# Kernel tuning notes

Measured on AMD Instinct MI355X. Metric: run time of the kernel, lower is better.

Reference implementation:

```python
import jax, jax.numpy as jnp
import numpy as np

HIDDEN = 512
NHEADS = 8
ALPHA = 0.1
NUM_HOP = 4
MASK_VAL = -16384.0
LN_EPS = 1e-5


def setup_inputs() -> dict:
    key = jax.random.key(0)
    ks = jax.random.split(key, 10)
    B, N, H = 8, 1024, HIDDEN
    s = 1.0 / np.sqrt(H)
    x = jax.random.normal(ks[0], (B, N, H), dtype=jnp.float32)
    adj = jax.random.randint(ks[1], (B, N, N), 0, 2, dtype=jnp.int32)
    Wq = jax.random.uniform(ks[2], (H, H), jnp.float32, -s, s)
    bq = jax.random.uniform(ks[3], (H,), jnp.float32, -s, s)
    Wk = jax.random.uniform(ks[4], (H, H), jnp.float32, -s, s)
    bk = jax.random.uniform(ks[5], (H,), jnp.float32, -s, s)
    Wv = jax.random.uniform(ks[6], (H, H), jnp.float32, -s, s)
    bv = jax.random.uniform(ks[7], (H,), jnp.float32, -s, s)
    gamma = jnp.ones((H,), jnp.float32)
    beta = jnp.zeros((H,), jnp.float32)
    return {"x": x, "adj": adj, "Wq": Wq, "bq": bq, "Wk": Wk, "bk": bk,
            "Wv": Wv, "bv": bv, "gamma": gamma, "beta": beta}


def reference(x, adj, Wq, bq, Wk, bk, Wv, bv, gamma, beta):
    B, N, H = x.shape
    u = H // NHEADS
    # torch Linear: y = x @ W^T + b
    q = x @ Wq.T + bq  # [B,N,H]
    k = x @ Wk.T + bk
    v = x @ Wv.T + bv
    # split hidden into contiguous head chunks (matches per-head slicing)
    qh = q.reshape(B, N, NHEADS, u).transpose(0, 2, 1, 3)  # [B,Hd,N,u]
    kh = k.reshape(B, N, NHEADS, u).transpose(0, 2, 1, 3)
    vh = v.reshape(B, N, NHEADS, u).transpose(0, 2, 1, 3)
    scores = jnp.einsum('bhnd,bhmd->bhnm', qh, kh)  # [B,Hd,N,N]
    mask = (adj == 0)[:, None, :, :]  # broadcast over heads
    scores = jnp.where(mask, MASK_VAL, scores)
    pros = jax.nn.softmax(scores, axis=-1)
    z_init = vh
    z = z_init
    for _ in range(NUM_HOP):
        z = (1.0 - ALPHA) * jnp.einsum('bhnm,bhmd->bhnd', pros, z) + ALPHA * z_init
    h_prime = z.transpose(0, 2, 1, 3).reshape(B, N, H)  # concat heads
    y = x + h_prime
    mu = jnp.mean(y, axis=-1, keepdims=True)
    var = jnp.mean((y - mu) ** 2, axis=-1, keepdims=True)
    return (y - mu) / jnp.sqrt(var + LN_EPS) * gamma + beta
```

## Files before the change

### kernel.cpp

```cpp
#include <hip/hip_runtime.h>
#include <hip/hip_bf16.h>

#define BB 8
#define NN 1024
#define HH 512
#define NHEADS 8
#define UU 64

typedef __attribute__((ext_vector_type(8))) short short8;
typedef __attribute__((ext_vector_type(4))) float f32x4;
typedef __attribute__((ext_vector_type(16))) float f32x16;
typedef unsigned short u16;
typedef unsigned char u8;

__device__ inline float b2f(unsigned short u) {
    union { float f; unsigned int i; } c; c.i = ((unsigned int)u) << 16; return c.f;
}
__device__ inline unsigned short f2b(float f) {
    __hip_bfloat16 h = __float2bfloat16(f);
    return *reinterpret_cast<unsigned short*>(&h);
}
__device__ inline unsigned int pkbf(float a, float b) {
    union { float f; unsigned int u; } ca, cb; ca.f = a; cb.f = b;
    return ((ca.u + 0x8000u) >> 16) | ((cb.u + 0x8000u) & 0xffff0000u);
}
__device__ inline float upk_lo(unsigned int u) {
    union { float f; unsigned int i; } c; c.i = u << 16; return c.f;
}
__device__ inline float upk_hi(unsigned int u) {
    union { float f; unsigned int i; } c; c.i = u & 0xffff0000u; return c.f;
}
__device__ inline void gl_lds16(const void* g, void* l) {
    __builtin_amdgcn_global_load_lds(
        (const __attribute__((address_space(1))) unsigned int*)g,
        (__attribute__((address_space(3))) unsigned int*)l, 16, 0, 0);
}

__global__ __launch_bounds__(256) void cvt_w(
    const float* __restrict__ Wq, const float* __restrict__ Wk,
    const float* __restrict__ Wv, u16* __restrict__ Wb)
{
    const int which = blockIdx.y;
    const float* src = which == 0 ? Wq : (which == 1 ? Wk : Wv);
    u16* dst = Wb + (size_t)which * HH * HH;
    const int base = (blockIdx.x * 256 + threadIdx.x) * 8;
    const float4* sp = (const float4*)&src[base];
    float4 a = sp[0], b = sp[1];
    short8 o;
    o[0] = (short)f2b(a.x); o[1] = (short)f2b(a.y);
    o[2] = (short)f2b(a.z); o[3] = (short)f2b(a.w);
    o[4] = (short)f2b(b.x); o[5] = (short)f2b(b.y);
    o[6] = (short)f2b(b.z); o[7] = (short)f2b(b.w);
    *(short8*)&dst[base] = o;
}

__global__ __launch_bounds__(256) void adj_pack(
    const int* __restrict__ adj, unsigned int* __restrict__ adjpT)
{
    const int wave = threadIdx.x >> 6, lane = threadIdx.x & 63;
    const int row = blockIdx.x * 4 + wave;
    const int b = row >> 10, r = row & 1023;
    const int* ar = adj + (size_t)row * NN;
    unsigned int* ob = adjpT + (((size_t)b) << 15) + r;
    #pragma unroll
    for (int it = 0; it < 16; ++it) {
        int a = ar[it * 64 + lane];
        unsigned long long m = __ballot(a != 0);
        if (lane == 0) {
            ob[(size_t)(2 * it)     << 10] = (unsigned int)m;
            ob[(size_t)(2 * it + 1) << 10] = (unsigned int)(m >> 32);
        }
    }
}

__global__ __launch_bounds__(256) void qkv_gemm(
    const float* __restrict__ x, const u16* __restrict__ Wb,
    const float* __restrict__ bq, const float* __restrict__ bk,
    const float* __restrict__ bv,
    u16* __restrict__ q, u16* __restrict__ k, u16* __restrict__ v)
{
    const int which = blockIdx.z;
    const u16* W      = Wb + (size_t)which * HH * HH;
    const float* bias = which == 0 ? bq : (which == 1 ? bk : bv);
    u16* out          = which == 0 ? q  : (which == 1 ? k  : v);

    const int tid = threadIdx.x;
    const int wave = tid >> 6, lane = tid & 63;
    const int ln = lane & 15, quad = lane >> 4;
    const int wr = (wave >> 1) * 64, wc = (wave & 1) * 64;
    const int rowbase = blockIdx.x * 128, colbase = blockIdx.y * 128;

    __shared__ __align__(16) u16 As[128 * 40];
    __shared__ __align__(16) u16 Bs[128 * 32];
    __shared__ __align__(16) u16 Cs[128 * 136];

    f32x4 acc[4][4];
    #pragma unroll
    for (int ri = 0; ri < 4; ++ri)
        #pragma unroll
        for (int ci = 0; ci < 4; ++ci) acc[ri][ci] = (f32x4){0.f, 0.f, 0.f, 0.f};

    const int lr = lane >> 2;
    const int sg = lane & 3;

    for (int kk = 0; kk < HH; kk += 32) {
        __syncthreads();
        #pragma unroll
        for (int i = 0; i < 2; ++i) {
            int r = wave * 32 + i * 16 + lr;
            const float* xp = &x[(size_t)(rowbase + r) * HH + kk + sg * 8];
            float4 f0 = *(const float4*)xp, f1 = *(const float4*)(xp + 4);
            short8 o;
            o[0] = (short)f2b(f0.x); o[1] = (short)f2b(f0.y);
            o[2] = (short)f2b(f0.z); o[3] = (short)f2b(f0.w);
            o[4] = (short)f2b(f1.x); o[5] = (short)f2b(f1.y);
            o[6] = (short)f2b(f1.z); o[7] = (short)f2b(f1.w);
            *(short8*)&As[r * 40 + sg * 8] = o;
            gl_lds16(&W[(size_t)(colbase + r) * HH + kk + sg * 8],
                     (char*)Bs + (wave * 32 + i * 16) * 64);
        }
        __syncthreads();

        short8 bfr[4];
        #pragma unroll
        for (int ci = 0; ci < 4; ++ci)
            bfr[ci] = *(const short8*)&Bs[(wc + ci * 16 + ln) * 32 + quad * 8];
        #pragma unroll
        for (int ri = 0; ri < 4; ++ri) {
            short8 af = *(const short8*)&As[(wr + ri * 16 + ln) * 40 + quad * 8];
            #pragma unroll
            for (int ci = 0; ci < 4; ++ci)
                acc[ri][ci] = __builtin_amdgcn_mfma_f32_16x16x32_bf16(af, bfr[ci], acc[ri][ci], 0, 0, 0);
        }
    }

    #pragma unroll
    for (int ci = 0; ci < 4; ++ci) {
        int col = wc + ci * 16 + ln;
        float bb = bias[colbase + col];
        #pragma unroll
        for (int ri = 0; ri < 4; ++ri) {
            #pragma unroll
            for (int r = 0; r < 4; ++r) {
                int row = wr + ri * 16 + quad * 4 + r;
                Cs[row * 136 + col] = f2b(acc[ri][ci][r] + bb);
            }
        }
    }
    __syncthreads();
    {
        int row = tid >> 1, half = tid & 1;
        int gcol0 = colbase + half * 64;
        int hh = gcol0 >> 6;
        int grow = rowbase + row;
        int bidx = grow >> 10, n = grow & 1023;
        u16* op = &out[(((size_t)(bidx * NHEADS + hh)) * NN + n) * UU];
        const u16* cp = &Cs[row * 136 + half * 64];
        #pragma unroll
        for (int j = 0; j < 8; ++j)
            *(short8*)(op + j * 8) = *(const short8*)(cp + j * 8);
    }
}

__global__ __launch_bounds__(256) void vt8(
    const u16* __restrict__ v, u8* __restrict__ v8t)
{
    const int bh = blockIdx.x >> 2, part = blockIdx.x & 3;
    const int t = threadIdx.x;
    const size_t hd = (size_t)bh << 16;
    __shared__ u16 tile[64][72];

    for (int chunk = part * 4; chunk < part * 4 + 4; ++chunk) {
        const int n0 = chunk * 64;
        const int r = t >> 2, cs = t & 3;
        const u16* vp = &v[((size_t)bh * NN + n0 + r) * UU + cs * 16];
        short8 a = *(const short8*)vp;
        short8 b8 = *(const short8*)(vp + 8);
        #pragma unroll
        for (int j = 0; j < 8; ++j) {
            tile[r][cs * 16 + j] = (u16)a[j];
            tile[r][cs * 16 + 8 + j] = (u16)b8[j];
        }
        __syncthreads();
        const int c = t & 63, qt = t >> 6;
        unsigned int w[4];
        #pragma unroll
        for (int g = 0; g < 4; ++g) {
            float f0 = b2f(tile[qt * 16 + g * 4 + 0][c]);
            float f1 = b2f(tile[qt * 16 + g * 4 + 1][c]);
            float f2 = b2f(tile[qt * 16 + g * 4 + 2][c]);
            float f3 = b2f(tile[qt * 16 + g * 4 + 3][c]);
            int lo = __builtin_amdgcn_cvt_pk_fp8_f32(f0, f1, 0, false);
            w[g] = (unsigned int)__builtin_amdgcn_cvt_pk_fp8_f32(f2, f3, lo, true);
        }
        uint4 o; o.x = w[0]; o.y = w[1]; o.z = w[2]; o.w = w[3];
        *(uint4*)&v8t[hd + (size_t)c * 1024 + n0 + qt * 16] = o;
        __syncthreads();
    }
}

__device__ inline f32x16 score_tile(const u16* kp, const short8* qf)
{
    short8 kf[4];
    #pragma unroll
    for (int f = 0; f < 4; ++f) kf[f] = *(const short8*)(kp + f * 16);
    f32x16 acc;
    #pragma unroll
    for (int j = 0; j < 16; ++j) acc[j] = 0.f;
    #pragma unroll
    for (int f = 0; f < 4; ++f)
        acc = __builtin_amdgcn_mfma_f32_32x32x16_bf16(kf[f], qf[f], acc, 0, 0, 0);
    return acc;
}

__global__ __launch_bounds__(512, 4) void scores_softmax(
    const u16* __restrict__ q, const u16* __restrict__ kmat,
    const unsigned int* __restrict__ adjpT, u8* __restrict__ P8)
{
    const int gid = blockIdx.x;
    const int j = gid >> 3;
    const int h = gid & 7;
    const int b = j >> 5;
    const int bx = j & 31;
    const int bh = b * NHEADS + h;

    const int tid = threadIdx.x;
    const int kq = tid >> 6, lane = tid & 63;
    const int l31 = lane & 31, hi = lane >> 5;
    const int n = bx * 32 + l31;
    const int kt0 = kq * 4;

    __shared__ float rs[8][32];

    short8 qf[4];
    const u16* qp = &q[((size_t)bh * NN + n) * UU + hi * 8];
    #pragma unroll
    for (int f = 0; f < 4; ++f) qf[f] = *(const short8*)(qp + f * 16);

    const u16* kbase = kmat + (size_t)bh * NN * UU + (size_t)(kt0 * 32 + l31) * UU + hi * 8;
    const unsigned int* mbase = adjpT + (((size_t)b) << 15) + n;

    unsigned int mv[4];
    #pragma unroll
    for (int i = 0; i < 4; ++i)
        mv[i] = mbase[(size_t)(kt0 + i) << 10] >> (4 * hi);

    const float L2E = 1.442695041f;
    const float C0 = -46.16624f;
    const float CM = -100000.0f;

    unsigned int eb[4][4][2];
    float rs0 = 0.f, rs1 = 0.f, rs2 = 0.f, rs3 = 0.f;
    #pragma unroll
    for (int i = 0; i < 4; ++i) {
        f32x16 acc = score_tile(kbase + (size_t)i * (32 * UU), qf);
        const unsigned int m2 = mv[i];
        #pragma unroll
        for (int g = 0; g < 4; ++g) {
            float e[4];
            #pragma unroll
            for (int r = 0; r < 4; ++r) {
                const int koff = r + 8 * g;
                float addv = ((m2 >> koff) & 1u) ? C0 : CM;
                e[r] = __builtin_amdgcn_exp2f(fmaf(L2E, acc[g * 4 + r], addv));
            }
            if (g == 0) rs0 += (e[0] + e[1]) + (e[2] + e[3]);
            else if (g == 1) rs1 += (e[0] + e[1]) + (e[2] + e[3]);
            else if (g == 2) rs2 += (e[0] + e[1]) + (e[2] + e[3]);
            else rs3 += (e[0] + e[1]) + (e[2] + e[3]);
            eb[i][g][0] = pkbf(e[0], e[1]);
            eb[i][g][1] = pkbf(e[2], e[3]);
        }
    }
    float rsum = (rs0 + rs1) + (rs2 + rs3);
    rsum += __shfl_xor(rsum, 32);
    if (lane < 32) rs[kq][lane] = rsum;
    __syncthreads();
    const float total = ((rs[0][l31] + rs[1][l31]) + (rs[2][l31] + rs[3][l31]))
                      + ((rs[4][l31] + rs[5][l31]) + (rs[6][l31] + rs[7][l31]));
    const float scl = 16.0f / total;

    u8* pb = P8 + (((size_t)bh) << 20) + (size_t)(n >> 4) * 16384
           + (n & 15) * 32 + hi * 16;
    #pragma unroll
    for (int i = 0; i < 4; ++i) {
        unsigned int dw[4];
        #pragma unroll
        for (int g = 0; g < 4; ++g) {
            float e0 = upk_lo(eb[i][g][0]) * scl;
            float e1 = upk_hi(eb[i][g][0]) * scl;
            float e2 = upk_lo(eb[i][g][1]) * scl;
            float e3 = upk_hi(eb[i][g][1]) * scl;
            int lo = __builtin_amdgcn_cvt_pk_fp8_f32(e0, e1, 0, false);
            dw[g] = (unsigned int)__builtin_amdgcn_cvt_pk_fp8_f32(e2, e3, lo, true);
        }
        unsigned int sendA = hi ? dw[0] : dw[2];
        unsigned int sendB = hi ? dw[1] : dw[3];
        unsigned int recvA = (unsigned int)__shfl_xor((int)sendA, 32);
        unsigned int recvB = (unsigned int)__shfl_xor((int)sendB, 32);
        uint4 o;
        o.x = hi ? recvA : dw[0];
        o.y = hi ? dw[2] : recvA;
        o.z = hi ? recvB : dw[1];
        o.w = hi ? dw[3] : recvB;
        *(uint4*)(pb + (size_t)(kt0 + i) * 512) = o;
    }
}

__global__ __launch_bounds__(512) void hop(
    const u8* __restrict__ P8, const u8* __restrict__ z8in,
    const u16* __restrict__ v, u8* __restrict__ z8out,
    u16* __restrict__ zbf_out, int last)
{
    const int b = blockIdx.z, h = blockIdx.y, rt = blockIdx.x;
    const int bh = b * NHEADS + h;
    const int tid = threadIdx.x;
    const int wave = tid >> 6, lane = tid & 63;
    const int ln = lane & 15, quad = lane >> 4;
    const int wrow = rt * 128 + wave * 16;

    __shared__ __align__(16) u8 zt[64 * 1040];

    const u8* zg = z8in + ((size_t)bh << 16);
    #pragma unroll
    for (int i = 0; i < 8; ++i) {
        int c = wave * 8 + i;
        gl_lds16(zg + (size_t)c * 1024 + lane * 16, (char*)zt + c * 1040);
    }
    __syncthreads();

    f32x4 acc[4];
    #pragma unroll
    for (int ci = 0; ci < 4; ++ci) acc[ci] = (f32x4){0.f, 0.f, 0.f, 0.f};

    const u8* pt = P8 + ((size_t)bh << 20) + (size_t)(rt * 8 + wave) * 16384
                 + ln * 32 + quad * 8;
    #pragma unroll 4
    for (int kc = 0; kc < 32; ++kc) {
        long a = *(const long*)(pt + kc * 512);
        int kk = kc * 32;
        #pragma unroll
        for (int ci = 0; ci < 4; ++ci) {
            long bz = *(const long*)&zt[(ci * 16 + ln) * 1040 + kk + quad * 8];
            acc[ci] = __builtin_amdgcn_mfma_f32_16x16x32_fp8_fp8(a, bz, acc[ci], 0, 0, 0);
        }
    }

    if (last) {
        #pragma unroll
        for (int ci = 0; ci < 4; ++ci) {
            int col = ci * 16 + ln;
            #pragma unroll
            for (int r = 0; r < 4; ++r) {
                int row = wrow + quad * 4 + r;
                float vv = b2f(v[((size_t)bh * NN + row) * UU + col]);
                zbf_out[((size_t)(b * NN + row)) * HH + h * UU + col]
                    = f2b(0.05625f * acc[ci][r] + 0.1f * vv);
            }
        }
    } else {
        u8* zo = z8out + ((size_t)bh << 16);
        #pragma unroll
        for (int ci = 0; ci < 4; ++ci) {
            int col = ci * 16 + ln;
            float zv[4];
            #pragma unroll
            for (int r = 0; r < 4; ++r) {
                int row = wrow + quad * 4 + r;
                float vv = b2f(v[((size_t)bh * NN + row) * UU + col]);
                zv[r] = 0.05625f * acc[ci][r] + 0.1f * vv;
            }
            int lo = __builtin_amdgcn_cvt_pk_fp8_f32(zv[0], zv[1], 0, false);
            unsigned int dw = (unsigned int)__builtin_amdgcn_cvt_pk_fp8_f32(zv[2], zv[3], lo, true);
            *(unsigned int*)&zo[(size_t)col * 1024 + wrow + quad * 4] = dw;
        }
    }
}

__global__ __launch_bounds__(256) void resid_ln(
    const float* __restrict__ x, const u16* __restrict__ z,
    const float* __restrict__ gamma, const float* __restrict__ beta,
    float* __restrict__ out)
{
    const int r = blockIdx.x * 4 + (threadIdx.x >> 6);
    const int lane = threadIdx.x & 63;
    const size_t base = (size_t)r * HH + lane * 8;

    const float4* xp = (const float4*)&x[base];
    float4 x0 = xp[0], x1 = xp[1];
    short8 zv = *(const short8*)&z[base];
    float y[8];
    y[0] = x0.x + b2f((u16)zv[0]); y[1] = x0.y + b2f((u16)zv[1]);
    y[2] = x0.z + b2f((u16)zv[2]); y[3] = x0.w + b2f((u16)zv[3]);
    y[4] = x1.x + b2f((u16)zv[4]); y[5] = x1.y + b2f((u16)zv[5]);
    y[6] = x1.z + b2f((u16)zv[6]); y[7] = x1.w + b2f((u16)zv[7]);

    float s = 0.f, sq = 0.f;
    #pragma unroll
    for (int j = 0; j < 8; ++j) { s += y[j]; sq += y[j] * y[j]; }
    #pragma unroll
    for (int off = 32; off >= 1; off >>= 1) {
        s  += __shfl_xor(s, off);
        sq += __shfl_xor(sq, off);
    }
    const float mu = s * (1.0f / HH);
    const float var = sq * (1.0f / HH) - mu * mu;
    const float rstd = rsqrtf(var + 1e-5f);

    const float4* gp = (const float4*)&gamma[lane * 8];
    const float4* bp = (const float4*)&beta[lane * 8];
    float4 g0 = gp[0], g1 = gp[1], b0 = bp[0], b1 = bp[1];

    float4 o0, o1;
    o0.x = (y[0] - mu) * rstd * g0.x + b0.x;
    o0.y = (y[1] - mu) * rstd * g0.y + b0.y;
    o0.z = (y[2] - mu) * rstd * g0.z + b0.z;
    o0.w = (y[3] - mu) * rstd * g0.w + b0.w;
    o1.x = (y[4] - mu) * rstd * g1.x + b1.x;
    o1.y = (y[5] - mu) * rstd * g1.y + b1.y;
    o1.z = (y[6] - mu) * rstd * g1.z + b1.z;
    o1.w = (y[7] - mu) * rstd * g1.w + b1.w;
    float4* op = (float4*)&out[base];
    op[0] = o0; op[1] = o1;
}

extern "C" void kernel_launch(void* const* d_in, const int* in_sizes, int n_in,
                              void* d_out, int out_size, void* d_ws, size_t ws_size,
                              hipStream_t stream)
{
    const float* x   = (const float*)d_in[0];
    const int* adj   = (const int*)d_in[1];
    const float* Wq  = (const float*)d_in[2];
    const float* bq  = (const float*)d_in[3];
    const float* Wk  = (const float*)d_in[4];
    const float* bk  = (const float*)d_in[5];
    const float* Wv  = (const float*)d_in[6];
    const float* bv  = (const float*)d_in[7];
    const float* gamma = (const float*)d_in[8];
    const float* beta  = (const float*)d_in[9];
    float* out = (float*)d_out;

    const size_t E = (size_t)BB * NN * HH;
    u16* ws16 = (u16*)d_ws;
    u16* q  = ws16 + E;
    u16* k  = ws16 + 2 * E;
    u16* v  = ws16 + 3 * E;
    u16* za = ws16 + 4 * E;
    u16* Wb = ws16 + 5 * E;
    u8* base8 = (u8*)(ws16 + 5 * E + 786432);
    u8* P8  = base8;
    u8* z8a = base8 + ((size_t)64 << 20);
    u8* z8b = z8a + ((size_t)4 << 20);
    u8* v8t = z8b + ((size_t)4 << 20);
    unsigned int* adjpT = (unsigned int*)(v8t + ((size_t)4 << 20));

    cvt_w<<<dim3(128, 3), 256, 0, stream>>>(Wq, Wk, Wv, Wb);
    adj_pack<<<dim3(2048), 256, 0, stream>>>(adj, adjpT);
    qkv_gemm<<<dim3(64, 4, 3), 256, 0, stream>>>(x, Wb, bq, bk, bv, q, k, v);
    vt8<<<dim3(256), 256, 0, stream>>>(v, v8t);
    scores_softmax<<<dim3(2048), 512, 0, stream>>>(q, k, adjpT, P8);
    hop<<<dim3(8, NHEADS, BB), 512, 0, stream>>>(P8, v8t, v, z8a, za, 0);
    hop<<<dim3(8, NHEADS, BB), 512, 0, stream>>>(P8, z8a, v, z8b, za, 0);
    hop<<<dim3(8, NHEADS, BB), 512, 0, stream>>>(P8, z8b, v, z8a, za, 0);
    hop<<<dim3(8, NHEADS, BB), 512, 0, stream>>>(P8, z8a, v, z8b, za, 1);
    resid_ln<<<dim3(2048), 256, 0, stream>>>(x, za, gamma, beta, out);
}
```

Measured before the change: 268.3 us.

## Pre-convert x to bf16, prefetch P8 in hop loop, use packed bf16 cvt

Adds a separate kernel that converts x to bf16 once, so qkv_gemm can load its A tiles straight into LDS with global_load_lds. Before, every column block re-read and re-converted fp32 x. The hop kernel now prefetches the first four P8 fragments before the barrier and keeps a rotating four-deep register prefetch, so global loads overlap the MFMAs. pkbf now uses the v_cvt_pk_bf16_f32 instruction. The cost is one extra launch plus a write and re-read of bf16 x, and pkbf's rounding changes from add-and-truncate to the hardware conversion.

```diff
diff --git a/kernel.cpp b/kernel.cpp
--- a/kernel.cpp
+++ b/kernel.cpp
@@ -21,8 +21,9 @@
     return *reinterpret_cast<unsigned short*>(&h);
 }
 __device__ inline unsigned int pkbf(float a, float b) {
-    union { float f; unsigned int u; } ca, cb; ca.f = a; cb.f = b;
-    return ((ca.u + 0x8000u) >> 16) | ((cb.u + 0x8000u) & 0xffff0000u);
+    unsigned int r;
+    asm("v_cvt_pk_bf16_f32 %0, %1, %2" : "=v"(r) : "v"(a), "v"(b));
+    return r;
 }
 __device__ inline float upk_lo(unsigned int u) {
     union { float f; unsigned int i; } c; c.i = u << 16; return c.f;
@@ -54,6 +55,20 @@
     *(short8*)&dst[base] = o;
 }
 
+__global__ __launch_bounds__(256) void cvt_x(
+    const float* __restrict__ x, u16* __restrict__ xb)
+{
+    const int base = (blockIdx.x * 256 + threadIdx.x) * 8;
+    const float4* sp = (const float4*)&x[base];
+    float4 a = sp[0], b = sp[1];
+    short8 o;
+    o[0] = (short)f2b(a.x); o[1] = (short)f2b(a.y);
+    o[2] = (short)f2b(a.z); o[3] = (short)f2b(a.w);
+    o[4] = (short)f2b(b.x); o[5] = (short)f2b(b.y);
+    o[6] = (short)f2b(b.z); o[7] = (short)f2b(b.w);
+    *(short8*)&xb[base] = o;
+}
+
 __global__ __launch_bounds__(256) void adj_pack(
     const int* __restrict__ adj, unsigned int* __restrict__ adjpT)
 {
@@ -74,7 +89,7 @@
 }
 
 __global__ __launch_bounds__(256) void qkv_gemm(
-    const float* __restrict__ x, const u16* __restrict__ Wb,
+    const u16* __restrict__ xb, const u16* __restrict__ Wb,
     const float* __restrict__ bq, const float* __restrict__ bk,
     const float* __restrict__ bv,
     u16* __restrict__ q, u16* __restrict__ k, u16* __restrict__ v)
@@ -90,7 +105,7 @@
     const int wr = (wave >> 1) * 64, wc = (wave & 1) * 64;
     const int rowbase = blockIdx.x * 128, colbase = blockIdx.y * 128;
 
-    __shared__ __align__(16) u16 As[128 * 40];
+    __shared__ __align__(16) u16 As[128 * 32];
     __shared__ __align__(16) u16 Bs[128 * 32];
     __shared__ __align__(16) u16 Cs[128 * 136];
 
@@ -108,14 +123,8 @@
         #pragma unroll
         for (int i = 0; i < 2; ++i) {
             int r = wave * 32 + i * 16 + lr;
-            const float* xp = &x[(size_t)(rowbase + r) * HH + kk + sg * 8];
-            float4 f0 = *(const float4*)xp, f1 = *(const float4*)(xp + 4);
-            short8 o;
-            o[0] = (short)f2b(f0.x); o[1] = (short)f2b(f0.y);
-            o[2] = (short)f2b(f0.z); o[3] = (short)f2b(f0.w);
-            o[4] = (short)f2b(f1.x); o[5] = (short)f2b(f1.y);
-            o[6] = (short)f2b(f1.z); o[7] = (short)f2b(f1.w);
-            *(short8*)&As[r * 40 + sg * 8] = o;
+            gl_lds16(&xb[(size_t)(rowbase + r) * HH + kk + sg * 8],
+                     (char*)As + (wave * 32 + i * 16) * 64);
             gl_lds16(&W[(size_t)(colbase + r) * HH + kk + sg * 8],
                      (char*)Bs + (wave * 32 + i * 16) * 64);
         }
@@ -127,7 +136,7 @@
             bfr[ci] = *(const short8*)&Bs[(wc + ci * 16 + ln) * 32 + quad * 8];
         #pragma unroll
         for (int ri = 0; ri < 4; ++ri) {
-            short8 af = *(const short8*)&As[(wr + ri * 16 + ln) * 40 + quad * 8];
+            short8 af = *(const short8*)&As[(wr + ri * 16 + ln) * 32 + quad * 8];
             #pragma unroll
             for (int ci = 0; ci < 4; ++ci)
                 acc[ri][ci] = __builtin_amdgcn_mfma_f32_16x16x32_bf16(af, bfr[ci], acc[ri][ci], 0, 0, 0);
@@ -327,17 +336,23 @@
         int c = wave * 8 + i;
         gl_lds16(zg + (size_t)c * 1024 + lane * 16, (char*)zt + c * 1040);
     }
-    __syncthreads();
-
-    f32x4 acc[4];
-    #pragma unroll
-    for (int ci = 0; ci < 4; ++ci) acc[ci] = (f32x4){0.f, 0.f, 0.f, 0.f};
 
     const u8* pt = P8 + ((size_t)bh << 20) + (size_t)(rt * 8 + wave) * 16384
                  + ln * 32 + quad * 8;
-    #pragma unroll 4
+    long pa[4];
+    #pragma unroll
+    for (int i = 0; i < 4; ++i) pa[i] = *(const long*)(pt + i * 512);
+
+    __syncthreads();
+
+    f32x4 acc[4];
+    #pragma unroll
+    for (int ci = 0; ci < 4; ++ci) acc[ci] = (f32x4){0.f, 0.f, 0.f, 0.f};
+
+    #pragma unroll
     for (int kc = 0; kc < 32; ++kc) {
-        long a = *(const long*)(pt + kc * 512);
+        long a = pa[kc & 3];
+        if (kc + 4 < 32) pa[kc & 3] = *(const long*)(pt + (kc + 4) * 512);
         int kk = kc * 32;
         #pragma unroll
         for (int ci = 0; ci < 4; ++ci) {
@@ -442,6 +457,7 @@
 
     const size_t E = (size_t)BB * NN * HH;
     u16* ws16 = (u16*)d_ws;
+    u16* xb = ws16;
     u16* q  = ws16 + E;
     u16* k  = ws16 + 2 * E;
     u16* v  = ws16 + 3 * E;
@@ -454,9 +470,10 @@
     u8* v8t = z8b + ((size_t)4 << 20);
     unsigned int* adjpT = (unsigned int*)(v8t + ((size_t)4 << 20));
 
+    cvt_x<<<dim3(2048), 256, 0, stream>>>(x, xb);
     cvt_w<<<dim3(128, 3), 256, 0, stream>>>(Wq, Wk, Wv, Wb);
     adj_pack<<<dim3(2048), 256, 0, stream>>>(adj, adjpT);
-    qkv_gemm<<<dim3(64, 4, 3), 256, 0, stream>>>(x, Wb, bq, bk, bv, q, k, v);
+    qkv_gemm<<<dim3(64, 4, 3), 256, 0, stream>>>(xb, Wb, bq, bk, bv, q, k, v);
     vt8<<<dim3(256), 256, 0, stream>>>(v, v8t);
     scores_softmax<<<dim3(2048), 512, 0, stream>>>(q, k, adjpT, P8);
     hop<<<dim3(8, NHEADS, BB), 512, 0, stream>>>(P8, v8t, v, z8a, za, 0);
```

Result: no change. 270.6 us (+0.8%).
